# Performance work log

Hardware: AMD Instinct MI355X
Metric: run time of the kernel (lower is better)

Reference implementation:

```python
import jax, jax.numpy as jnp
import numpy as np

# Material constants (from init_kwargs: E=1e4, nu=0.3)
E_MOD = 1.0e4
NU = 0.3
MU = E_MOD / (2.0 * (1.0 + NU))                      # shear modulus
LMBDA = E_MOD * NU / ((1.0 + NU) * (1.0 - 2.0 * NU))  # first Lame parameter
EPS = 1e-10

B, N_NODES, N_ELEM, N_QUAD, NPE = 4, 100000, 500000, 4, 4  # tet4 mesh


def setup_inputs() -> dict:
    key = jax.random.key(0)
    k1, k2, k3, k4 = jax.random.split(key, 4)
    # small displacements so J = det(I + grad_u) stays positive
    u = jax.random.normal(k1, (B, N_NODES, 3), dtype=jnp.float32) * 0.01
    elements = jax.random.randint(k2, (N_ELEM, NPE), 0, N_NODES)
    # precomputed shape-function derivatives dN/dx per element/quad point
    dN_dx = jax.random.normal(k3, (N_ELEM, N_QUAD, NPE, 3), dtype=jnp.float32) * 0.1
    # positive Jacobian determinants of the reference->physical map
    detJ = jax.random.uniform(k4, (N_ELEM, N_QUAD), dtype=jnp.float32, minval=0.5, maxval=1.5) * 1e-3
    # tet4 4-point quadrature weights: 0.25 / 6
    quad_weights = jnp.full((N_QUAD,), 0.25 / 6.0, dtype=jnp.float32)
    return {"u": u, "elements": elements, "dN_dx": dN_dx, "detJ": detJ,
            "quad_weights": quad_weights}


def reference(u, elements, dN_dx, detJ, quad_weights):
    # gather nodal displacements per element: [B, E, n, 3]
    elem_u = u[:, elements]
    # grad_u[b,e,q,i,j] = sum_n elem_u[b,e,n,i] * dN_dx[e,q,n,j]  -> [B,E,Q,3,3]
    grad_u = jnp.einsum('beni,eqnj->beqij', elem_u, dN_dx)
    F = grad_u + jnp.eye(3, dtype=u.dtype)
    J = jnp.linalg.det(F)                      # [B,E,Q]
    I_C = jnp.sum(F * F, axis=(-2, -1))        # tr(F^T F)
    logJ = jnp.log(jnp.maximum(J, EPS))
    W = 0.5 * MU * (I_C - 3.0 - 2.0 * logJ) + 0.25 * LMBDA * (J * J - 1.0 - 2.0 * logJ)
    # quadrature-weighted assembly over elements and quad points -> [B]
    return jnp.einsum('beq,eq,q->b', W, detJ, quad_weights)
```

## Files before the change

### kernel.cpp

```cpp
#include <hip/hip_runtime.h>

#define MU_C   3846.1538461538462f
#define LM_C   5769.2307692307695f
#define EPS_C  1e-10f

#define ELB 64
#define SLAB 52

__global__ __launch_bounds__(256) void nh_transpose_u_pad(
    const float* __restrict__ u, float4* __restrict__ ut, int n_nodes)
{
    const int i = blockIdx.x * 256 + threadIdx.x;
    if (i >= n_nodes) return;
    float4* q = ut + (size_t)i * 4;
    #pragma unroll
    for (int b = 0; b < 4; ++b) {
        const float* p = u + ((size_t)b * n_nodes + i) * 3;
        q[b] = make_float4(p[0], p[1], p[2], 0.f);
    }
}

__global__ __launch_bounds__(256) void nh_partial_v3(
    const float* __restrict__ u,
    const float4* __restrict__ ut,
    const int*   __restrict__ elements,
    const float* __restrict__ dN_dx,
    const float* __restrict__ detJ,
    const float* __restrict__ qw,
    float* __restrict__ partial,
    int n_elem, int n_nodes, int use_ut)
{
    __shared__ float s_dn[ELB * SLAB];
    __shared__ int   s_el[ELB * 4];
    __shared__ float s_dj[ELB * 4];
    __shared__ float s_red[4][4];

    const int t  = threadIdx.x;
    const int e0 = blockIdx.x * ELB;
    const int rem = min(ELB, n_elem - e0);

    {
        const float4* src = reinterpret_cast<const float4*>(dN_dx) + (size_t)e0 * 12;
        const int nf4 = rem * 12;
        #pragma unroll
        for (int j = 0; j < 3; ++j) {
            const int m = t + 256 * j;
            if (m < nf4) {
                const float4 v = src[m];
                const int el = m / 12, ch = m % 12;
                *reinterpret_cast<float4*>(&s_dn[el * SLAB + ch * 4]) = v;
            }
        }
    }
    if (t < 64) {
        if (t < rem)
            reinterpret_cast<int4*>(s_el)[t] =
                reinterpret_cast<const int4*>(elements)[e0 + t];
    } else if (t < 128) {
        const int i = t - 64;
        if (i < rem)
            reinterpret_cast<float4*>(s_dj)[i] =
                reinterpret_cast<const float4*>(detJ)[e0 + i];
    }
    __syncthreads();

    const int el = t >> 2;
    const int b  = t & 3;
    float a = 0.f;

    if (el < rem) {
        const int4 nd = reinterpret_cast<const int4*>(s_el)[el];
        const int nodes[4] = {nd.x, nd.y, nd.z, nd.w};

        float eu[4][3];
        if (use_ut) {
            #pragma unroll
            for (int n = 0; n < 4; ++n) {
                const float4 v = ut[(size_t)nodes[n] * 4 + b];
                eu[n][0] = v.x; eu[n][1] = v.y; eu[n][2] = v.z;
            }
        } else {
            const float* ub = u + (size_t)b * n_nodes * 3;
            #pragma unroll
            for (int n = 0; n < 4; ++n) {
                const float* p = ub + (size_t)nodes[n] * 3;
                eu[n][0] = p[0]; eu[n][1] = p[1]; eu[n][2] = p[2];
            }
        }

        const float4 w4 = *reinterpret_cast<const float4*>(qw);
        const float* dj = &s_dj[el * 4];
        const float wq[4] = {dj[0] * w4.x, dj[1] * w4.y, dj[2] * w4.z, dj[3] * w4.w};

        const float* slab = &s_dn[el * SLAB];
        #pragma unroll
        for (int q = 0; q < 4; ++q) {
            float4 f0 = *reinterpret_cast<const float4*>(slab + q * 12 + 0);
            float4 f1 = *reinterpret_cast<const float4*>(slab + q * 12 + 4);
            float4 f2 = *reinterpret_cast<const float4*>(slab + q * 12 + 8);
            float d[12] = {f0.x, f0.y, f0.z, f0.w, f1.x, f1.y, f1.z, f1.w,
                           f2.x, f2.y, f2.z, f2.w};

            float F[3][3];
            #pragma unroll
            for (int i = 0; i < 3; ++i) {
                #pragma unroll
                for (int j = 0; j < 3; ++j) {
                    float g = 0.f;
                    #pragma unroll
                    for (int n = 0; n < 4; ++n)
                        g = fmaf(eu[n][i], d[n * 3 + j], g);
                    F[i][j] = g + ((i == j) ? 1.f : 0.f);
                }
            }
            const float J =
                  F[0][0] * (F[1][1]*F[2][2] - F[1][2]*F[2][1])
                - F[0][1] * (F[1][0]*F[2][2] - F[1][2]*F[2][0])
                + F[0][2] * (F[1][0]*F[2][1] - F[1][1]*F[2][0]);

            float IC = 0.f;
            #pragma unroll
            for (int i = 0; i < 3; ++i)
                #pragma unroll
                for (int j = 0; j < 3; ++j)
                    IC = fmaf(F[i][j], F[i][j], IC);

            const float lj = __logf(fmaxf(J, EPS_C));
            const float W = 0.5f * MU_C * (IC - 3.f - 2.f * lj)
                          + 0.25f * LM_C * (fmaf(J, J, -1.f) - 2.f * lj);
            a = fmaf(W, wq[q], a);
        }
    }

    #pragma unroll
    for (int off = 32; off >= 4; off >>= 1)
        a += __shfl_down(a, off);

    const int lane = t & 63;
    const int wid  = t >> 6;
    if (lane < 4) s_red[wid][lane] = a;
    __syncthreads();
    if (t < 4)
        partial[(size_t)blockIdx.x * 4 + t] =
            (s_red[0][t] + s_red[1][t]) + (s_red[2][t] + s_red[3][t]);
}

__global__ __launch_bounds__(256) void nh_final(
    const float* __restrict__ partial,
    float* __restrict__ out,
    int nparts)
{
    float accb[4] = {0.f, 0.f, 0.f, 0.f};
    for (int i = threadIdx.x; i < nparts; i += 256) {
        const float4 p = reinterpret_cast<const float4*>(partial)[i];
        accb[0] += p.x; accb[1] += p.y; accb[2] += p.z; accb[3] += p.w;
    }

    #pragma unroll
    for (int b = 0; b < 4; ++b) {
        float v = accb[b];
        #pragma unroll
        for (int off = 32; off > 0; off >>= 1)
            v += __shfl_down(v, off);
        accb[b] = v;
    }

    __shared__ float lds[4][4];
    const int lane = threadIdx.x & 63;
    const int wid  = threadIdx.x >> 6;
    if (lane == 0) {
        #pragma unroll
        for (int b = 0; b < 4; ++b) lds[wid][b] = accb[b];
    }
    __syncthreads();
    if (threadIdx.x == 0) {
        #pragma unroll
        for (int b = 0; b < 4; ++b)
            out[b] = (lds[0][b] + lds[1][b]) + (lds[2][b] + lds[3][b]);
    }
}

extern "C" void kernel_launch(void* const* d_in, const int* in_sizes, int n_in,
                              void* d_out, int out_size, void* d_ws, size_t ws_size,
                              hipStream_t stream) {
    const float* u        = (const float*)d_in[0];
    const int*   elements = (const int*)d_in[1];
    const float* dN_dx    = (const float*)d_in[2];
    const float* detJ     = (const float*)d_in[3];
    const float* qw       = (const float*)d_in[4];
    float* out = (float*)d_out;

    const int B       = out_size;
    const int n_nodes = in_sizes[0] / (3 * B);
    const int n_elem  = in_sizes[1] / 4;

    const int threads = 256;
    const int nblocks = (n_elem + ELB - 1) / ELB;

    const size_t ut_bytes      = (size_t)n_nodes * 4 * sizeof(float4);
    const size_t partial_bytes = (size_t)nblocks * 4 * sizeof(float);
    const int use_ut = (ws_size >= ut_bytes + partial_bytes) ? 1 : 0;

    float4* ut     = (float4*)d_ws;
    float* partial = use_ut ? (float*)((char*)d_ws + ut_bytes) : (float*)d_ws;

    if (use_ut) {
        const int tb = (n_nodes + threads - 1) / threads;
        nh_transpose_u_pad<<<tb, threads, 0, stream>>>(u, ut, n_nodes);
    }

    nh_partial_v3<<<nblocks, threads, 0, stream>>>(u, ut, elements, dN_dx, detJ, qw,
                                                   partial, n_elem, n_nodes, use_ut);
    nh_final<<<1, threads, 0, stream>>>(partial, out, nblocks);
}
```

Before: 59.97 us.

## Map one element per thread handling all batches, with transposed LDS dN_dx layout

Each thread now processes one element for all four batch entries instead of one element-batch pair, so each block covers 256 elements. dN_dx is staged in LDS in a quad-chunk-major (structure-of-arrays) layout for conflict-free float4 reads, and element indices and detJ are loaded directly from global memory. The log terms are algebraically merged into a single coefficient. The aim is to amortize dN_dx reads and index loads across batches and cut the number of blocks and partials. The cost is higher register pressure, since each thread holds 48 displacement values, plus 48KB of LDS per block, which may reduce occupancy.

```diff
diff --git a/kernel.cpp b/kernel.cpp
--- a/kernel.cpp
+++ b/kernel.cpp
@@ -2,10 +2,10 @@
 
 #define MU_C   3846.1538461538462f
 #define LM_C   5769.2307692307695f
+#define LOGC   (MU_C + 0.5f * LM_C)
 #define EPS_C  1e-10f
 
-#define ELB 64
-#define SLAB 52
+#define ELB 256
 
 __global__ __launch_bounds__(256) void nh_transpose_u_pad(
     const float* __restrict__ u, float4* __restrict__ ut, int n_nodes)
@@ -20,7 +20,7 @@
     }
 }
 
-__global__ __launch_bounds__(256) void nh_partial_v3(
+__global__ __launch_bounds__(256) void nh_partial_v4(
     const float* __restrict__ u,
     const float4* __restrict__ ut,
     const int*   __restrict__ elements,
@@ -30,115 +30,118 @@
     float* __restrict__ partial,
     int n_elem, int n_nodes, int use_ut)
 {
-    __shared__ float s_dn[ELB * SLAB];
-    __shared__ int   s_el[ELB * 4];
-    __shared__ float s_dj[ELB * 4];
-    __shared__ float s_red[4][4];
-
-    const int t  = threadIdx.x;
-    const int e0 = blockIdx.x * ELB;
+    __shared__ float4 s_dn4[12 * ELB];
+    __shared__ float  s_red[4][4];
+
+    const int t   = threadIdx.x;
+    const int e0  = blockIdx.x * ELB;
     const int rem = min(ELB, n_elem - e0);
 
     {
         const float4* src = reinterpret_cast<const float4*>(dN_dx) + (size_t)e0 * 12;
         const int nf4 = rem * 12;
         #pragma unroll
-        for (int j = 0; j < 3; ++j) {
+        for (int j = 0; j < 12; ++j) {
             const int m = t + 256 * j;
             if (m < nf4) {
                 const float4 v = src[m];
-                const int el = m / 12, ch = m % 12;
-                *reinterpret_cast<float4*>(&s_dn[el * SLAB + ch * 4]) = v;
+                s_dn4[(m % 12) * ELB + (m / 12)] = v;
             }
         }
     }
-    if (t < 64) {
-        if (t < rem)
-            reinterpret_cast<int4*>(s_el)[t] =
-                reinterpret_cast<const int4*>(elements)[e0 + t];
-    } else if (t < 128) {
-        const int i = t - 64;
-        if (i < rem)
-            reinterpret_cast<float4*>(s_dj)[i] =
-                reinterpret_cast<const float4*>(detJ)[e0 + i];
-    }
     __syncthreads();
 
-    const int el = t >> 2;
-    const int b  = t & 3;
-    float a = 0.f;
-
-    if (el < rem) {
-        const int4 nd = reinterpret_cast<const int4*>(s_el)[el];
+    float acc[4] = {0.f, 0.f, 0.f, 0.f};
+
+    if (t < rem) {
+        const int e = e0 + t;
+        const int4 nd = reinterpret_cast<const int4*>(elements)[e];
         const int nodes[4] = {nd.x, nd.y, nd.z, nd.w};
 
-        float eu[4][3];
+        const float4 dj = reinterpret_cast<const float4*>(detJ)[e];
+        const float4 w4 = *reinterpret_cast<const float4*>(qw);
+        const float wq[4] = {dj.x * w4.x, dj.y * w4.y, dj.z * w4.z, dj.w * w4.w};
+
+        float eu[4][4][3];
         if (use_ut) {
             #pragma unroll
             for (int n = 0; n < 4; ++n) {
-                const float4 v = ut[(size_t)nodes[n] * 4 + b];
-                eu[n][0] = v.x; eu[n][1] = v.y; eu[n][2] = v.z;
+                const float4* p = ut + (size_t)nodes[n] * 4;
+                #pragma unroll
+                for (int b = 0; b < 4; ++b) {
+                    const float4 v = p[b];
+                    eu[n][b][0] = v.x; eu[n][b][1] = v.y; eu[n][b][2] = v.z;
+                }
             }
         } else {
-            const float* ub = u + (size_t)b * n_nodes * 3;
             #pragma unroll
             for (int n = 0; n < 4; ++n) {
-                const float* p = ub + (size_t)nodes[n] * 3;
-                eu[n][0] = p[0]; eu[n][1] = p[1]; eu[n][2] = p[2];
+                #pragma unroll
+                for (int b = 0; b < 4; ++b) {
+                    const float* p = u + ((size_t)b * n_nodes + nodes[n]) * 3;
+                    eu[n][b][0] = p[0]; eu[n][b][1] = p[1]; eu[n][b][2] = p[2];
+                }
             }
         }
 
-        const float4 w4 = *reinterpret_cast<const float4*>(qw);
-        const float* dj = &s_dj[el * 4];
-        const float wq[4] = {dj[0] * w4.x, dj[1] * w4.y, dj[2] * w4.z, dj[3] * w4.w};
-
-        const float* slab = &s_dn[el * SLAB];
         #pragma unroll
         for (int q = 0; q < 4; ++q) {
-            float4 f0 = *reinterpret_cast<const float4*>(slab + q * 12 + 0);
-            float4 f1 = *reinterpret_cast<const float4*>(slab + q * 12 + 4);
-            float4 f2 = *reinterpret_cast<const float4*>(slab + q * 12 + 8);
-            float d[12] = {f0.x, f0.y, f0.z, f0.w, f1.x, f1.y, f1.z, f1.w,
-                           f2.x, f2.y, f2.z, f2.w};
-
-            float F[3][3];
+            const float4 f0 = s_dn4[(q * 3 + 0) * ELB + t];
+            const float4 f1 = s_dn4[(q * 3 + 1) * ELB + t];
+            const float4 f2 = s_dn4[(q * 3 + 2) * ELB + t];
+            const float d[12] = {f0.x, f0.y, f0.z, f0.w, f1.x, f1.y, f1.z, f1.w,
+                                 f2.x, f2.y, f2.z, f2.w};
+
             #pragma unroll
-            for (int i = 0; i < 3; ++i) {
-                #pragma unroll
-                for (int j = 0; j < 3; ++j) {
-                    float g = 0.f;
+            for (int b = 0; b < 4; ++b) {
+                float F[3][3];
+                #pragma unroll
+                for (int i = 0; i < 3; ++i) {
                     #pragma unroll
-                    for (int n = 0; n < 4; ++n)
-                        g = fmaf(eu[n][i], d[n * 3 + j], g);
-                    F[i][j] = g + ((i == j) ? 1.f : 0.f);
+                    for (int j = 0; j < 3; ++j) {
+                        float g = 0.f;
+                        #pragma unroll
+                        for (int n = 0; n < 4; ++n)
+                            g = fmaf(eu[n][b][i], d[n * 3 + j], g);
+                        F[i][j] = g + ((i == j) ? 1.f : 0.f);
+                    }
                 }
-            }
-            const float J =
-                  F[0][0] * (F[1][1]*F[2][2] - F[1][2]*F[2][1])
-                - F[0][1] * (F[1][0]*F[2][2] - F[1][2]*F[2][0])
-                + F[0][2] * (F[1][0]*F[2][1] - F[1][1]*F[2][0]);
-
-            float IC = 0.f;
-            #pragma unroll
-            for (int i = 0; i < 3; ++i)
-                #pragma unroll
-                for (int j = 0; j < 3; ++j)
-                    IC = fmaf(F[i][j], F[i][j], IC);
-
-            const float lj = __logf(fmaxf(J, EPS_C));
-            const float W = 0.5f * MU_C * (IC - 3.f - 2.f * lj)
-                          + 0.25f * LM_C * (fmaf(J, J, -1.f) - 2.f * lj);
-            a = fmaf(W, wq[q], a);
+                const float J =
+                      F[0][0] * (F[1][1]*F[2][2] - F[1][2]*F[2][1])
+                    - F[0][1] * (F[1][0]*F[2][2] - F[1][2]*F[2][0])
+                    + F[0][2] * (F[1][0]*F[2][1] - F[1][1]*F[2][0]);
+
+                float IC = 0.f;
+                #pragma unroll
+                for (int i = 0; i < 3; ++i)
+                    #pragma unroll
+                    for (int j = 0; j < 3; ++j)
+                        IC = fmaf(F[i][j], F[i][j], IC);
+
+                const float lj = __logf(fmaxf(J, EPS_C));
+                const float W = 0.5f * MU_C * (IC - 3.f)
+                              + 0.25f * LM_C * fmaf(J, J, -1.f)
+                              - LOGC * lj;
+                acc[b] = fmaf(W, wq[q], acc[b]);
+            }
         }
     }
 
     #pragma unroll
-    for (int off = 32; off >= 4; off >>= 1)
-        a += __shfl_down(a, off);
+    for (int b = 0; b < 4; ++b) {
+        float v = acc[b];
+        #pragma unroll
+        for (int off = 32; off > 0; off >>= 1)
+            v += __shfl_down(v, off);
+        acc[b] = v;
+    }
 
     const int lane = t & 63;
     const int wid  = t >> 6;
-    if (lane < 4) s_red[wid][lane] = a;
+    if (lane == 0) {
+        #pragma unroll
+        for (int b = 0; b < 4; ++b) s_red[wid][b] = acc[b];
+    }
     __syncthreads();
     if (t < 4)
         partial[(size_t)blockIdx.x * 4 + t] =
@@ -209,7 +212,7 @@
         nh_transpose_u_pad<<<tb, threads, 0, stream>>>(u, ut, n_nodes);
     }
 
-    nh_partial_v3<<<nblocks, threads, 0, stream>>>(u, ut, elements, dN_dx, detJ, qw,
+    nh_partial_v4<<<nblocks, threads, 0, stream>>>(u, ut, elements, dN_dx, detJ, qw,
                                                    partial, n_elem, n_nodes, use_ut);
     nh_final<<<1, threads, 0, stream>>>(partial, out, nblocks);
 }
```

Result: slower. 103.7 us (+73.0%).

## Replace LDS staging with direct nontemporal per-thread loads, two elements per thread

Applied to the files above, without the earlier changes.

Removes the shared-memory staging of dN_dx, connectivity and detJ. Each thread now loads its two elements' data directly with nontemporal vector loads and processes two elements per thread, so each block covers 128 elements. The log terms are also folded into a single constant. This drops the block barrier and LDS traffic, but the four batch lanes now fetch the same dN_dx data redundantly and the global loads are strided, and the extra live registers may reduce occupancy.

```diff
diff --git a/kernel.cpp b/kernel.cpp
--- a/kernel.cpp
+++ b/kernel.cpp
@@ -2,10 +2,13 @@
 
 #define MU_C   3846.1538461538462f
 #define LM_C   5769.2307692307695f
+#define LOGC   (MU_C + 0.5f * LM_C)
 #define EPS_C  1e-10f
 
-#define ELB 64
-#define SLAB 52
+typedef float nf4 __attribute__((ext_vector_type(4)));
+typedef int   ni4 __attribute__((ext_vector_type(4)));
+
+#define EPB 128
 
 __global__ __launch_bounds__(256) void nh_transpose_u_pad(
     const float* __restrict__ u, float4* __restrict__ ut, int n_nodes)
@@ -20,7 +23,47 @@
     }
 }
 
-__global__ __launch_bounds__(256) void nh_partial_v3(
+__device__ __forceinline__ float nh_energy_elem(
+    const nf4* __restrict__ dv,
+    const float eu[4][3],
+    const float wq[4])
+{
+    const float* d = reinterpret_cast<const float*>(dv);
+    float a = 0.f;
+    #pragma unroll
+    for (int q = 0; q < 4; ++q) {
+        float F[3][3];
+        #pragma unroll
+        for (int i = 0; i < 3; ++i) {
+            #pragma unroll
+            for (int j = 0; j < 3; ++j) {
+                float g = 0.f;
+                #pragma unroll
+                for (int n = 0; n < 4; ++n)
+                    g = fmaf(eu[n][i], d[(q*4 + n)*3 + j], g);
+                F[i][j] = g + ((i == j) ? 1.f : 0.f);
+            }
+        }
+        const float J =
+              F[0][0] * (F[1][1]*F[2][2] - F[1][2]*F[2][1])
+            - F[0][1] * (F[1][0]*F[2][2] - F[1][2]*F[2][0])
+            + F[0][2] * (F[1][0]*F[2][1] - F[1][1]*F[2][0]);
+        float IC = 0.f;
+        #pragma unroll
+        for (int i = 0; i < 3; ++i)
+            #pragma unroll
+            for (int j = 0; j < 3; ++j)
+                IC = fmaf(F[i][j], F[i][j], IC);
+        const float lj = __logf(fmaxf(J, EPS_C));
+        const float W = 0.5f * MU_C * (IC - 3.f)
+                      + 0.25f * LM_C * fmaf(J, J, -1.f)
+                      - LOGC * lj;
+        a = fmaf(W, wq[q], a);
+    }
+    return a;
+}
+
+__global__ __launch_bounds__(256) void nh_partial_v5(
     const float* __restrict__ u,
     const float4* __restrict__ ut,
     const int*   __restrict__ elements,
@@ -30,115 +73,82 @@
     float* __restrict__ partial,
     int n_elem, int n_nodes, int use_ut)
 {
-    __shared__ float s_dn[ELB * SLAB];
-    __shared__ int   s_el[ELB * 4];
-    __shared__ float s_dj[ELB * 4];
-    __shared__ float s_red[4][4];
-
     const int t  = threadIdx.x;
-    const int e0 = blockIdx.x * ELB;
-    const int rem = min(ELB, n_elem - e0);
-
-    {
-        const float4* src = reinterpret_cast<const float4*>(dN_dx) + (size_t)e0 * 12;
-        const int nf4 = rem * 12;
-        #pragma unroll
-        for (int j = 0; j < 3; ++j) {
-            const int m = t + 256 * j;
-            if (m < nf4) {
-                const float4 v = src[m];
-                const int el = m / 12, ch = m % 12;
-                *reinterpret_cast<float4*>(&s_dn[el * SLAB + ch * 4]) = v;
-            }
+    const int b  = t & 3;
+    const int p  = t >> 2;
+    const int e0 = blockIdx.x * EPB + p * 2;
+    const int e1 = e0 + 1;
+    const bool v0 = (e0 < n_elem);
+    const bool v1 = (e1 < n_elem);
+
+    const ni4* elp = reinterpret_cast<const ni4*>(elements);
+    const nf4* djp = reinterpret_cast<const nf4*>(detJ);
+    const nf4* dnp = reinterpret_cast<const nf4*>(dN_dx);
+
+    float acc = 0.f;
+
+    if (v0) {
+        ni4 nd0 = __builtin_nontemporal_load(elp + e0);
+        ni4 nd1; nd1 = v1 ? __builtin_nontemporal_load(elp + e1) : nd0;
+        nf4 dj0 = __builtin_nontemporal_load(djp + e0);
+        nf4 dj1; dj1 = v1 ? __builtin_nontemporal_load(djp + e1) : dj0;
+
+        nf4 dv0[12], dv1[12];
+        {
+            const nf4* p0 = dnp + (size_t)e0 * 12;
+            #pragma unroll
+            for (int k = 0; k < 12; ++k) dv0[k] = __builtin_nontemporal_load(p0 + k);
+            const nf4* p1 = dnp + (size_t)(v1 ? e1 : e0) * 12;
+            #pragma unroll
+            for (int k = 0; k < 12; ++k) dv1[k] = __builtin_nontemporal_load(p1 + k);
         }
-    }
-    if (t < 64) {
-        if (t < rem)
-            reinterpret_cast<int4*>(s_el)[t] =
-                reinterpret_cast<const int4*>(elements)[e0 + t];
-    } else if (t < 128) {
-        const int i = t - 64;
-        if (i < rem)
-            reinterpret_cast<float4*>(s_dj)[i] =
-                reinterpret_cast<const float4*>(detJ)[e0 + i];
-    }
-    __syncthreads();
-
-    const int el = t >> 2;
-    const int b  = t & 3;
-    float a = 0.f;
-
-    if (el < rem) {
-        const int4 nd = reinterpret_cast<const int4*>(s_el)[el];
-        const int nodes[4] = {nd.x, nd.y, nd.z, nd.w};
-
-        float eu[4][3];
+
+        float eu0[4][3], eu1[4][3];
         if (use_ut) {
-            #pragma unroll
-            for (int n = 0; n < 4; ++n) {
-                const float4 v = ut[(size_t)nodes[n] * 4 + b];
-                eu[n][0] = v.x; eu[n][1] = v.y; eu[n][2] = v.z;
+            const int* nd0p = (const int*)&nd0;
+            const int* nd1p = (const int*)&nd1;
+            #pragma unroll
+            for (int n = 0; n < 4; ++n) {
+                const float4 a4 = ut[(size_t)nd0p[n] * 4 + b];
+                eu0[n][0] = a4.x; eu0[n][1] = a4.y; eu0[n][2] = a4.z;
+            }
+            #pragma unroll
+            for (int n = 0; n < 4; ++n) {
+                const float4 a4 = ut[(size_t)nd1p[n] * 4 + b];
+                eu1[n][0] = a4.x; eu1[n][1] = a4.y; eu1[n][2] = a4.z;
             }
         } else {
             const float* ub = u + (size_t)b * n_nodes * 3;
-            #pragma unroll
-            for (int n = 0; n < 4; ++n) {
-                const float* p = ub + (size_t)nodes[n] * 3;
-                eu[n][0] = p[0]; eu[n][1] = p[1]; eu[n][2] = p[2];
+            const int* nd0p = (const int*)&nd0;
+            const int* nd1p = (const int*)&nd1;
+            #pragma unroll
+            for (int n = 0; n < 4; ++n) {
+                const float* pp = ub + (size_t)nd0p[n] * 3;
+                eu0[n][0] = pp[0]; eu0[n][1] = pp[1]; eu0[n][2] = pp[2];
+            }
+            #pragma unroll
+            for (int n = 0; n < 4; ++n) {
+                const float* pp = ub + (size_t)nd1p[n] * 3;
+                eu1[n][0] = pp[0]; eu1[n][1] = pp[1]; eu1[n][2] = pp[2];
             }
         }
 
         const float4 w4 = *reinterpret_cast<const float4*>(qw);
-        const float* dj = &s_dj[el * 4];
-        const float wq[4] = {dj[0] * w4.x, dj[1] * w4.y, dj[2] * w4.z, dj[3] * w4.w};
-
-        const float* slab = &s_dn[el * SLAB];
-        #pragma unroll
-        for (int q = 0; q < 4; ++q) {
-            float4 f0 = *reinterpret_cast<const float4*>(slab + q * 12 + 0);
-            float4 f1 = *reinterpret_cast<const float4*>(slab + q * 12 + 4);
-            float4 f2 = *reinterpret_cast<const float4*>(slab + q * 12 + 8);
-            float d[12] = {f0.x, f0.y, f0.z, f0.w, f1.x, f1.y, f1.z, f1.w,
-                           f2.x, f2.y, f2.z, f2.w};
-
-            float F[3][3];
-            #pragma unroll
-            for (int i = 0; i < 3; ++i) {
-                #pragma unroll
-                for (int j = 0; j < 3; ++j) {
-                    float g = 0.f;
-                    #pragma unroll
-                    for (int n = 0; n < 4; ++n)
-                        g = fmaf(eu[n][i], d[n * 3 + j], g);
-                    F[i][j] = g + ((i == j) ? 1.f : 0.f);
-                }
-            }
-            const float J =
-                  F[0][0] * (F[1][1]*F[2][2] - F[1][2]*F[2][1])
-                - F[0][1] * (F[1][0]*F[2][2] - F[1][2]*F[2][0])
-                + F[0][2] * (F[1][0]*F[2][1] - F[1][1]*F[2][0]);
-
-            float IC = 0.f;
-            #pragma unroll
-            for (int i = 0; i < 3; ++i)
-                #pragma unroll
-                for (int j = 0; j < 3; ++j)
-                    IC = fmaf(F[i][j], F[i][j], IC);
-
-            const float lj = __logf(fmaxf(J, EPS_C));
-            const float W = 0.5f * MU_C * (IC - 3.f - 2.f * lj)
-                          + 0.25f * LM_C * (fmaf(J, J, -1.f) - 2.f * lj);
-            a = fmaf(W, wq[q], a);
-        }
+        const float wq0[4] = {dj0.x * w4.x, dj0.y * w4.y, dj0.z * w4.z, dj0.w * w4.w};
+        const float wq1[4] = {dj1.x * w4.x, dj1.y * w4.y, dj1.z * w4.z, dj1.w * w4.w};
+
+        acc = nh_energy_elem(dv0, eu0, wq0);
+        if (v1) acc += nh_energy_elem(dv1, eu1, wq1);
     }
 
     #pragma unroll
     for (int off = 32; off >= 4; off >>= 1)
-        a += __shfl_down(a, off);
-
+        acc += __shfl_down(acc, off);
+
+    __shared__ float s_red[4][4];
     const int lane = t & 63;
     const int wid  = t >> 6;
-    if (lane < 4) s_red[wid][lane] = a;
+    if (lane < 4) s_red[wid][lane] = acc;
     __syncthreads();
     if (t < 4)
         partial[(size_t)blockIdx.x * 4 + t] =
@@ -195,7 +205,7 @@
     const int n_elem  = in_sizes[1] / 4;
 
     const int threads = 256;
-    const int nblocks = (n_elem + ELB - 1) / ELB;
+    const int nblocks = (n_elem + EPB - 1) / EPB;
 
     const size_t ut_bytes      = (size_t)n_nodes * 4 * sizeof(float4);
     const size_t partial_bytes = (size_t)nblocks * 4 * sizeof(float);
@@ -209,7 +219,7 @@
         nh_transpose_u_pad<<<tb, threads, 0, stream>>>(u, ut, n_nodes);
     }
 
-    nh_partial_v3<<<nblocks, threads, 0, stream>>>(u, ut, elements, dN_dx, detJ, qw,
+    nh_partial_v5<<<nblocks, threads, 0, stream>>>(u, ut, elements, dN_dx, detJ, qw,
                                                    partial, n_elem, n_nodes, use_ut);
     nh_final<<<1, threads, 0, stream>>>(partial, out, nblocks);
 }
```

Result: slower. 90.54 us (+51.0%).
